# Kernel optimization log

Hardware: AMD Instinct MI355X
Metric: run time of the kernel (lower is better)

## Reference

```python
import jax, jax.numpy as jnp
from jax import lax
import numpy as np

N_PATTS, D_PATTS, L_PATTS = 64, 16, 64
L_OUT = L_PATTS  # module sets l_out = l_patts in both branches
RHO = 0.1
W = RHO ** (1.0 / L_PATTS)  # per-step decay weight
BIG = 1e30  # stands in for +inf at DP boundaries (avoids inf*0 nans)


def _dtw_matrix(x, patts, w):
    """Weighted-DTW DP matrix.
    x: (B, d, T), patts: (P, d, L) -> D: (B, P, L, T)
    D[i,j] = dist[i,j] + w * min(D[i-1,j], D[i,j-1], D[i-1,j-1]),
    with out-of-range predecessors = +inf and D[0,0] = dist[0,0].
    dist is the euclidean distance between x[:, :, j] and patts[:, :, i].
    """
    B, d, T = x.shape
    P, _, L = patts.shape
    x2 = jnp.sum(x * x, axis=1)              # (B, T)
    p2 = jnp.sum(patts * patts, axis=1)      # (P, L)
    xp = jnp.einsum('bdt,pdl->btpl', x, patts)  # (B, T, P, L)
    sq = x2[:, :, None, None] + p2[None, None, :, :] - 2.0 * xp
    dist = jnp.sqrt(jnp.maximum(sq, 1e-12))  # (B, T, P, L)
    dist_t = jnp.transpose(dist, (1, 0, 2, 3))  # (T, B, P, L) scan over time

    def col_step(prev_col, d_col):
        # prev_col = D[:, j-1] of shape (B, P, L); d_col = dist column (B, P, L)
        shifted = jnp.concatenate(
            [jnp.full_like(prev_col[..., :1], BIG), prev_col[..., :-1]], axis=-1)
        c = jnp.minimum(prev_col, shifted)  # min(D[i,j-1], D[i-1,j-1]) per i

        def cell(d_prev, inp):
            dist_i, c_i = inp              # each (B, P)
            m = jnp.minimum(d_prev, c_i)   # min over the 3 predecessors
            val = dist_i + jnp.where(m >= BIG * 0.5, 0.0, w * m)
            return val, val

        init = jnp.full(prev_col.shape[:2], BIG, prev_col.dtype)  # D[-1, j]
        _, col = lax.scan(
            cell, init,
            (jnp.moveaxis(d_col, -1, 0), jnp.moveaxis(c, -1, 0)))  # over i
        col = jnp.moveaxis(col, 0, -1)  # (B, P, L)
        return col, col

    init_col = jnp.full((B, P, L), BIG, dist.dtype)  # D[:, -1] = inf
    _, cols = lax.scan(col_step, init_col, dist_t)   # (T, B, P, L)
    return jnp.transpose(cols, (1, 2, 3, 0))         # (B, P, L, T)


def setup_inputs() -> dict:
    key = jax.random.key(0)
    kx, kp = jax.random.split(key)
    x = jax.random.normal(kx, (16, D_PATTS, 1024), dtype=jnp.float32)
    patts = jax.random.normal(kp, (N_PATTS, D_PATTS, L_PATTS), dtype=jnp.float32)
    return {"x": x, "patts": patts}


def reference(x, patts):
    D = _dtw_matrix(x, patts, W)          # (B, P, L, T)
    return D[:, :, :, -L_OUT:]            # last l_out time steps
```

## Files before the change

### kernel.cpp

```cpp
#include <hip/hip_runtime.h>
#include <math.h>

typedef _Float16 half8 __attribute__((ext_vector_type(8)));
typedef _Float16 h2 __attribute__((ext_vector_type(2)));
typedef float    f32x4 __attribute__((ext_vector_type(4)));
typedef unsigned int u32;
typedef unsigned long long u64;
typedef unsigned short u16;

#define BIGV 1e30f
#define RSTR 37

__device__ __forceinline__ u32 dpp_shr1(u32 oldv, u32 src) {
  return (u32)__builtin_amdgcn_update_dpp((int)oldv, (int)src, 0x138, 0xF, 0xF, false);
}
__device__ __forceinline__ float cvtlo(u32 v) {
  union { u16 u; _Float16 h; } c; c.u = (u16)v; return (float)c.h;
}
__device__ __forceinline__ u16 f2h(float f) {
  union { _Float16 h; u16 u; } c; c.h = (_Float16)f; return c.u;
}
__device__ __forceinline__ u32 pkrtz(float a, float b) {
  auto v = __builtin_amdgcn_cvt_pkrtz(a, b);
  union { decltype(v) h; u32 u; } c; c.h = v; return c.u;
}
__device__ __forceinline__ u32 funnel16(u32 hi, u32 lo, u32 sh) {
  return (u32)(((((u64)hi) << 32) | (u64)lo) >> sh);
}
__device__ __forceinline__ h2 as_h2(u32 u) { union { u32 u; h2 h; } x; x.u = u; return x.h; }

__global__ __launch_bounds__(512) void dtw_pc2(
    const float* __restrict__ x,
    const float* __restrict__ patts,
    float* __restrict__ out,
    float w) {
  __shared__ uint4 xsq[2050];
  __shared__ uint2 ring2[4 * 64 * RSTR];
  __shared__ float obuf[4 * 1024];
  __shared__ u16   x2h16[1024];

  const int tid = threadIdx.x, lane = tid & 63, wv = tid >> 6;
  const int b = blockIdx.x >> 4, pg = blockIdx.x & 15;
  const int role = wv >> 2, pr = wv & 3;
  const int p = pg * 4 + pr;
  const int le = lane & 15, kq = lane >> 4;

  {
    const float* xb = x + b * (16 * 1024);
    u16* xh = (u16*)xsq;
    for (int idx = tid; idx < 16384; idx += 512) {
      int d = idx >> 10, t = idx & 1023;
      xh[t * 16 + d] = f2h(xb[idx]);
    }
    if (tid == 0) { xsq[2048] = make_uint4(0,0,0,0); xsq[2049] = make_uint4(0,0,0,0); }
    __syncthreads();
    for (int t = tid; t < 1024; t += 512) {
      uint4 a0 = xsq[2 * t], a1 = xsq[2 * t + 1];
      float s2 = __builtin_amdgcn_fdot2(as_h2(a0.x), as_h2(a0.x), 0.f, false);
      s2 = __builtin_amdgcn_fdot2(as_h2(a0.y), as_h2(a0.y), s2, false);
      s2 = __builtin_amdgcn_fdot2(as_h2(a0.z), as_h2(a0.z), s2, false);
      s2 = __builtin_amdgcn_fdot2(as_h2(a0.w), as_h2(a0.w), s2, false);
      s2 = __builtin_amdgcn_fdot2(as_h2(a1.x), as_h2(a1.x), s2, false);
      s2 = __builtin_amdgcn_fdot2(as_h2(a1.y), as_h2(a1.y), s2, false);
      s2 = __builtin_amdgcn_fdot2(as_h2(a1.z), as_h2(a1.z), s2, false);
      s2 = __builtin_amdgcn_fdot2(as_h2(a1.w), as_h2(a1.w), s2, false);
      x2h16[t] = f2h(s2);
    }
  }
  __syncthreads();

  if (role == 0) {
    half8 bf[4];
    {
      const float* pp = patts + p * (16 * 64);
#pragma unroll
      for (int nb = 0; nb < 4; ++nb) {
        float pv[8]; float part = 0.f;
#pragma unroll
        for (int j = 0; j < 8; ++j) {
          float f = (kq < 2) ? pp[(8 * kq + j) * 64 + nb * 16 + le] : 0.f;
          pv[j] = f; part = fmaf(f, f, part);
        }
        part += __shfl_xor(part, 16, 64);
        part += __shfl_xor(part, 32, 64);
        u32 wd0 = pkrtz(-2.f * pv[0], -2.f * pv[1]);
        u32 wd1 = pkrtz(-2.f * pv[2], -2.f * pv[3]);
        u32 wd2 = pkrtz(-2.f * pv[4], -2.f * pv[5]);
        u32 wd3 = pkrtz(-2.f * pv[6], -2.f * pv[7]);
        if (kq == 2) { wd0 = 0x3C00u | ((u32)f2h(part) << 16); wd1 = 0; wd2 = 0; wd3 = 0; }
        union { uint4 q; half8 h; } bu; bu.q = make_uint4(wd0, wd1, wd2, wd3);
        bf[nb] = bu.h;
      }
    }
    int colp = 8 * kq;
    const int wpbase = pr * (64 * RSTR) + RSTR * le;

#define PRODUCE(T0) { \
    int aidx_ = (kq < 2) ? (2 * ((T0) + le) + kq) : 2048; \
    uint4 aq_ = xsq[aidx_]; \
    u32 x2b_ = (u32)x2h16[(T0) + le]; \
    aq_.x = (kq == 2) ? (x2b_ | 0x3C000000u) : aq_.x; \
    union { uint4 q; half8 h; } au_; au_.q = aq_; \
    int wb_ = wpbase + (colp >> 3); \
    bool mir_ = colp < 32; \
    _Pragma("unroll") \
    for (int nb_ = 0; nb_ < 4; ++nb_) { \
      f32x4 c_ = {0.f, 0.f, 0.f, 0.f}; \
      c_ = __builtin_amdgcn_mfma_f32_16x16x32_f16(au_.h, bf[nb_], c_, 0, 0, 0); \
      float d0_ = __builtin_amdgcn_sqrtf(fmaxf(c_[0], 1e-12f)); \
      float d1_ = __builtin_amdgcn_sqrtf(fmaxf(c_[1], 1e-12f)); \
      float d2_ = __builtin_amdgcn_sqrtf(fmaxf(c_[2], 1e-12f)); \
      float d3_ = __builtin_amdgcn_sqrtf(fmaxf(c_[3], 1e-12f)); \
      uint2 st_; st_.x = pkrtz(d0_, d1_); st_.y = pkrtz(d2_, d3_); \
      ring2[wb_ + (16 * RSTR) * nb_] = st_; \
      if (mir_) ring2[wb_ + (16 * RSTR) * nb_ + 32] = st_; \
    } \
    colp = (colp + 32) & 255; }

    PRODUCE(0); PRODUCE(16); PRODUCE(32); PRODUCE(48);
    __syncthreads();
#pragma unroll 1
    for (int k = 0; k < 30; ++k) {
      PRODUCE(32 * k + 64);
      PRODUCE(32 * k + 80);
      __syncthreads();
    }
    __syncthreads(); __syncthreads(); __syncthreads(); __syncthreads();

  } else {
    const int rcbase = pr * (64 * RSTR) + RSTR * lane;
    int colc = (((0 - lane) >> 2) << 3) & 255;
    const int ph = (0 - lane) & 3;
    const u32 shv = (u32)((ph & 1) * 16);
    const bool sel2 = (ph & 2) != 0;
    float prev = BIGV, shA = BIGV, shB = BIGV;
    const int bigbits = __float_as_int(BIGV);
    float* obf = obuf + pr * 1024;
    float* obw = obf + lane * 16;
    float* oprow = out + ((b * 64 + p) * 64 + lane) * 64;
    int nextq = 240;

#define LOADQ(Q0,Q1,Q2,Q3,Q4) { int ci_ = rcbase + (colc >> 3); \
    Q0 = ring2[ci_];     Q1 = ring2[ci_ + 1]; Q2 = ring2[ci_ + 2]; \
    Q3 = ring2[ci_ + 3]; Q4 = ring2[ci_ + 4]; \
    colc = (colc + 32) & 255; }

#define SHIFT(curv) { shB = shA; \
    shA = __int_as_float((int)dpp_shr1((u32)bigbits, (u32)__float_as_int(curv))); \
    prev = (curv); }

#define STEP_PRO(S, D) { float dist_ = (D); \
    float m_ = fminf(fminf(prev, shA), shB); \
    float ms_ = (m_ >= 0.5e30f) ? 0.f : m_; \
    float val_ = fmaf(w, ms_, dist_); \
    int t_ = (S) - lane; float cur_ = (t_ >= 0) ? val_ : BIGV; \
    SHIFT(cur_); }

#define STEP_MAIN(S, D) { float dist_ = (D); \
    float m_ = fminf(fminf(prev, shA), shB); \
    float cur_ = fmaf(w, m_, dist_); \
    SHIFT(cur_); }

#define STEP_EPI(S, D) { float dist_ = (D); \
    float m_ = fminf(fminf(prev, shA), shB); \
    float val_ = fmaf(w, m_, dist_); \
    int t_ = (S) - lane; float cur_ = (t_ <= 1023) ? val_ : BIGV; \
    if ((u32)(t_ - 960) < 64u) obw[t_ & 15] = val_; \
    SHIFT(cur_); }

#define FLUSHQ(SQ) { \
    if (nextq < 256 && 4 * nextq + 3 <= (SQ) - 1 - lane - 4) { \
      float4 v_ = *(const float4*)&obf[lane * 16 + ((nextq & 3) << 2)]; \
      *(float4*)(oprow + (nextq << 2) - 960) = v_; ++nextq; \
    } }

#define EXTRACT8(Q0, Q1, Q2, Q3, Q4) \
    u32 W0_ = sel2 ? Q0.y : Q0.x, W1_ = sel2 ? Q1.x : Q0.y, \
        W2_ = sel2 ? Q1.y : Q1.x, W3_ = sel2 ? Q2.x : Q1.y, \
        W4_ = sel2 ? Q2.y : Q2.x, W5_ = sel2 ? Q3.x : Q2.y, \
        W6_ = sel2 ? Q3.y : Q3.x, W7_ = sel2 ? Q4.x : Q3.y, \
        W8_ = sel2 ? Q4.y : Q4.x; \
    u32 A0 = funnel16(W1_, W0_, shv), A1 = funnel16(W2_, W1_, shv), \
        A2 = funnel16(W3_, W2_, shv), A3 = funnel16(W4_, W3_, shv), \
        A4 = funnel16(W5_, W4_, shv), A5 = funnel16(W6_, W5_, shv), \
        A6 = funnel16(W7_, W6_, shv), A7 = funnel16(W8_, W7_, shv);

#define S16(S0, STP) \
    STP((S0)+0,  cvtlo(A0)); STP((S0)+1,  cvtlo(A0 >> 16)); \
    STP((S0)+2,  cvtlo(A1)); STP((S0)+3,  cvtlo(A1 >> 16)); \
    STP((S0)+4,  cvtlo(A2)); STP((S0)+5,  cvtlo(A2 >> 16)); \
    STP((S0)+6,  cvtlo(A3)); STP((S0)+7,  cvtlo(A3 >> 16)); \
    STP((S0)+8,  cvtlo(A4)); STP((S0)+9,  cvtlo(A4 >> 16)); \
    STP((S0)+10, cvtlo(A5)); STP((S0)+11, cvtlo(A5 >> 16)); \
    STP((S0)+12, cvtlo(A6)); STP((S0)+13, cvtlo(A6 >> 16)); \
    STP((S0)+14, cvtlo(A7)); STP((S0)+15, cvtlo(A7 >> 16));

#define SET_PRO(S0)  S16(S0, STEP_PRO)
#define SET_MAIN(S0) S16(S0, STEP_MAIN)
#define SET_EPI(S0) \
    FLUSHQ((S0)+0);  STEP_EPI((S0)+0,  cvtlo(A0)); STEP_EPI((S0)+1,  cvtlo(A0 >> 16)); \
                     STEP_EPI((S0)+2,  cvtlo(A1)); STEP_EPI((S0)+3,  cvtlo(A1 >> 16)); \
    FLUSHQ((S0)+4);  STEP_EPI((S0)+4,  cvtlo(A2)); STEP_EPI((S0)+5,  cvtlo(A2 >> 16)); \
                     STEP_EPI((S0)+6,  cvtlo(A3)); STEP_EPI((S0)+7,  cvtlo(A3 >> 16)); \
    FLUSHQ((S0)+8);  STEP_EPI((S0)+8,  cvtlo(A4)); STEP_EPI((S0)+9,  cvtlo(A4 >> 16)); \
                     STEP_EPI((S0)+10, cvtlo(A5)); STEP_EPI((S0)+11, cvtlo(A5 >> 16)); \
    FLUSHQ((S0)+12); STEP_EPI((S0)+12, cvtlo(A6)); STEP_EPI((S0)+13, cvtlo(A6 >> 16)); \
                     STEP_EPI((S0)+14, cvtlo(A7)); STEP_EPI((S0)+15, cvtlo(A7 >> 16));

#define PHASE(C0,C1,C2,C3,C4,C5,C6,C7,C8,C9, L0,L1,L2,L3,L4,L5,L6,L7,L8,L9, S0, SETM) { \
    LOADQ(L0,L1,L2,L3,L4); LOADQ(L5,L6,L7,L8,L9); \
    { EXTRACT8(C0,C1,C2,C3,C4); SETM(S0); } \
    { EXTRACT8(C5,C6,C7,C8,C9); SETM((S0)+16); } \
    __syncthreads(); }

    __syncthreads();
    uint2 a0,a1,a2,a3,a4,a5,a6,a7,a8,a9;
    uint2 b0,b1,b2,b3,b4,b5,b6,b7,b8,b9;
    LOADQ(a0,a1,a2,a3,a4); LOADQ(a5,a6,a7,a8,a9);

    PHASE(a0,a1,a2,a3,a4,a5,a6,a7,a8,a9, b0,b1,b2,b3,b4,b5,b6,b7,b8,b9, 0,  SET_PRO);
    PHASE(b0,b1,b2,b3,b4,b5,b6,b7,b8,b9, a0,a1,a2,a3,a4,a5,a6,a7,a8,a9, 32, SET_PRO);
#pragma unroll 1
    for (int j = 1; j < 15; ++j) {
      PHASE(a0,a1,a2,a3,a4,a5,a6,a7,a8,a9, b0,b1,b2,b3,b4,b5,b6,b7,b8,b9, 64*j,      SET_MAIN);
      PHASE(b0,b1,b2,b3,b4,b5,b6,b7,b8,b9, a0,a1,a2,a3,a4,a5,a6,a7,a8,a9, 64*j + 32, SET_MAIN);
    }
    PHASE(a0,a1,a2,a3,a4,a5,a6,a7,a8,a9, b0,b1,b2,b3,b4,b5,b6,b7,b8,b9, 960,  SET_EPI);
    PHASE(b0,b1,b2,b3,b4,b5,b6,b7,b8,b9, a0,a1,a2,a3,a4,a5,a6,a7,a8,a9, 992,  SET_EPI);
    PHASE(a0,a1,a2,a3,a4,a5,a6,a7,a8,a9, b0,b1,b2,b3,b4,b5,b6,b7,b8,b9, 1024, SET_EPI);
    PHASE(b0,b1,b2,b3,b4,b5,b6,b7,b8,b9, a0,a1,a2,a3,a4,a5,a6,a7,a8,a9, 1056, SET_EPI);

#pragma unroll
    for (int rr = 0; rr < 4; ++rr) {
      if (nextq < 256) {
        float4 v_ = *(const float4*)&obf[lane * 16 + ((nextq & 3) << 2)];
        *(float4*)(oprow + (nextq << 2) - 960) = v_; ++nextq;
      }
    }
  }
}

extern "C" void kernel_launch(void* const* d_in, const int* in_sizes, int n_in,
                              void* d_out, int out_size, void* d_ws, size_t ws_size,
                              hipStream_t stream) {
  const float* x     = (const float*)d_in[0];
  const float* patts = (const float*)d_in[1];
  float* out         = (float*)d_out;
  const float w = (float)exp(log(0.1) / 64.0);
  dim3 grid(256), block(512);
  hipLaunchKernelGGL(dtw_pc2, grid, block, 0, stream, x, patts, out, w);
}
```

Baseline: 44.77 us.

## Process two DTW rows per lane with pair-packed ring layout

Restructures the consumer wavefront so each lane advances two time steps per DP step on an anti-diagonal. The ring buffer is re-laid-out as a byte-addressed row-pair ring with wraparound pointers, which removes the funnel-shift and select extraction. Output is now written directly to global memory instead of being staged through an LDS obuf, and plain barriers replace syncthreads. This is meant to cut ALU and LDS overhead per cell and halve the number of phases. The cost is a longer dependent chain per step and a larger ring footprint in LDS.

```diff
diff --git a/kernel.cpp b/kernel.cpp
--- a/kernel.cpp
+++ b/kernel.cpp
@@ -5,11 +5,9 @@
 typedef _Float16 h2 __attribute__((ext_vector_type(2)));
 typedef float    f32x4 __attribute__((ext_vector_type(4)));
 typedef unsigned int u32;
-typedef unsigned long long u64;
 typedef unsigned short u16;
 
 #define BIGV 1e30f
-#define RSTR 37
 
 __device__ __forceinline__ u32 dpp_shr1(u32 oldv, u32 src) {
   return (u32)__builtin_amdgcn_update_dpp((int)oldv, (int)src, 0x138, 0xF, 0xF, false);
@@ -24,20 +22,16 @@
   auto v = __builtin_amdgcn_cvt_pkrtz(a, b);
   union { decltype(v) h; u32 u; } c; c.h = v; return c.u;
 }
-__device__ __forceinline__ u32 funnel16(u32 hi, u32 lo, u32 sh) {
-  return (u32)(((((u64)hi) << 32) | (u64)lo) >> sh);
-}
 __device__ __forceinline__ h2 as_h2(u32 u) { union { u32 u; h2 h; } x; x.u = u; return x.h; }
 
-__global__ __launch_bounds__(512) void dtw_pc2(
+__global__ __launch_bounds__(512) void dtw_pc3(
     const float* __restrict__ x,
     const float* __restrict__ patts,
     float* __restrict__ out,
-    float w) {
+    float wd) {
   __shared__ uint4 xsq[2050];
-  __shared__ uint2 ring2[4 * 64 * RSTR];
-  __shared__ float obuf[4 * 1024];
   __shared__ u16   x2h16[1024];
+  __shared__ uint2 ring2[4 * 64 * 57];
 
   const int tid = threadIdx.x, lane = tid & 63, wv = tid >> 6;
   const int b = blockIdx.x >> 4, pg = blockIdx.x & 15;
@@ -92,8 +86,15 @@
         bf[nb] = bu.h;
       }
     }
-    int colp = 8 * kq;
-    const int wpbase = pr * (64 * RSTR) + RSTR * le;
+    u32 Aa[4], Ee[4];
+    const u32 pairbase = (u32)(pr * 29184);
+#pragma unroll
+    for (int nb = 0; nb < 4; ++nb) {
+      int row = nb * 16 + le;
+      u32 rb = pairbase + (u32)(row * 456);
+      Aa[nb] = rb + (u32)(4 * (2 * kq + (row & ~1)));
+      Ee[nb] = rb + 448u;
+    }
 
 #define PRODUCE(T0) { \
     int aidx_ = (kq < 2) ? (2 * ((T0) + le) + kq) : 2048; \
@@ -101,8 +102,6 @@
     u32 x2b_ = (u32)x2h16[(T0) + le]; \
     aq_.x = (kq == 2) ? (x2b_ | 0x3C000000u) : aq_.x; \
     union { uint4 q; half8 h; } au_; au_.q = aq_; \
-    int wb_ = wpbase + (colp >> 3); \
-    bool mir_ = colp < 32; \
     _Pragma("unroll") \
     for (int nb_ = 0; nb_ < 4; ++nb_) { \
       f32x4 c_ = {0.f, 0.f, 0.f, 0.f}; \
@@ -112,10 +111,9 @@
       float d2_ = __builtin_amdgcn_sqrtf(fmaxf(c_[2], 1e-12f)); \
       float d3_ = __builtin_amdgcn_sqrtf(fmaxf(c_[3], 1e-12f)); \
       uint2 st_; st_.x = pkrtz(d0_, d1_); st_.y = pkrtz(d2_, d3_); \
-      ring2[wb_ + (16 * RSTR) * nb_] = st_; \
-      if (mir_) ring2[wb_ + (16 * RSTR) * nb_ + 32] = st_; \
-    } \
-    colp = (colp + 32) & 255; }
+      *(uint2*)((char*)ring2 + Aa[nb_]) = st_; \
+      Aa[nb_] += 32u; if (Aa[nb_] >= Ee[nb_]) Aa[nb_] -= 448u; \
+    } }
 
     PRODUCE(0); PRODUCE(16); PRODUCE(32); PRODUCE(48);
     __syncthreads();
@@ -125,118 +123,81 @@
       PRODUCE(32 * k + 80);
       __syncthreads();
     }
-    __syncthreads(); __syncthreads(); __syncthreads(); __syncthreads();
+    for (int k = 0; k < 6; ++k) __syncthreads();
 
   } else {
-    const int rcbase = pr * (64 * RSTR) + RSTR * lane;
-    int colc = (((0 - lane) >> 2) << 3) & 255;
-    const int ph = (0 - lane) & 3;
-    const u32 shv = (u32)((ph & 1) * 16);
-    const bool sel2 = (ph & 2) != 0;
-    float prev = BIGV, shA = BIGV, shB = BIGV;
+    char* crow = (char*)ring2 + pr * 29184 + lane * 456;
+    u32 cb = 0;
+    const bool oddl = (lane & 1) != 0;
+    float prevB = BIGV, sA = BIGV, sB = BIGV, sBo = BIGV;
     const int bigbits = __float_as_int(BIGV);
-    float* obf = obuf + pr * 1024;
-    float* obw = obf + lane * 16;
     float* oprow = out + ((b * 64 + p) * 64 + lane) * 64;
-    int nextq = 240;
-
-#define LOADQ(Q0,Q1,Q2,Q3,Q4) { int ci_ = rcbase + (colc >> 3); \
-    Q0 = ring2[ci_];     Q1 = ring2[ci_ + 1]; Q2 = ring2[ci_ + 2]; \
-    Q3 = ring2[ci_ + 3]; Q4 = ring2[ci_ + 4]; \
-    colc = (colc + 32) & 255; }
-
-#define SHIFT(curv) { shB = shA; \
-    shA = __int_as_float((int)dpp_shr1((u32)bigbits, (u32)__float_as_int(curv))); \
-    prev = (curv); }
-
-#define STEP_PRO(S, D) { float dist_ = (D); \
-    float m_ = fminf(fminf(prev, shA), shB); \
-    float ms_ = (m_ >= 0.5e30f) ? 0.f : m_; \
-    float val_ = fmaf(w, ms_, dist_); \
-    int t_ = (S) - lane; float cur_ = (t_ >= 0) ? val_ : BIGV; \
-    SHIFT(cur_); }
-
-#define STEP_MAIN(S, D) { float dist_ = (D); \
-    float m_ = fminf(fminf(prev, shA), shB); \
-    float cur_ = fmaf(w, m_, dist_); \
-    SHIFT(cur_); }
-
-#define STEP_EPI(S, D) { float dist_ = (D); \
-    float m_ = fminf(fminf(prev, shA), shB); \
-    float val_ = fmaf(w, m_, dist_); \
-    int t_ = (S) - lane; float cur_ = (t_ <= 1023) ? val_ : BIGV; \
-    if ((u32)(t_ - 960) < 64u) obw[t_ & 15] = val_; \
-    SHIFT(cur_); }
-
-#define FLUSHQ(SQ) { \
-    if (nextq < 256 && 4 * nextq + 3 <= (SQ) - 1 - lane - 4) { \
-      float4 v_ = *(const float4*)&obf[lane * 16 + ((nextq & 3) << 2)]; \
-      *(float4*)(oprow + (nextq << 2) - 960) = v_; ++nextq; \
-    } }
-
-#define EXTRACT8(Q0, Q1, Q2, Q3, Q4) \
-    u32 W0_ = sel2 ? Q0.y : Q0.x, W1_ = sel2 ? Q1.x : Q0.y, \
-        W2_ = sel2 ? Q1.y : Q1.x, W3_ = sel2 ? Q2.x : Q1.y, \
-        W4_ = sel2 ? Q2.y : Q2.x, W5_ = sel2 ? Q3.x : Q2.y, \
-        W6_ = sel2 ? Q3.y : Q3.x, W7_ = sel2 ? Q4.x : Q3.y, \
-        W8_ = sel2 ? Q4.y : Q4.x; \
-    u32 A0 = funnel16(W1_, W0_, shv), A1 = funnel16(W2_, W1_, shv), \
-        A2 = funnel16(W3_, W2_, shv), A3 = funnel16(W4_, W3_, shv), \
-        A4 = funnel16(W5_, W4_, shv), A5 = funnel16(W6_, W5_, shv), \
-        A6 = funnel16(W7_, W6_, shv), A7 = funnel16(W8_, W7_, shv);
-
-#define S16(S0, STP) \
-    STP((S0)+0,  cvtlo(A0)); STP((S0)+1,  cvtlo(A0 >> 16)); \
-    STP((S0)+2,  cvtlo(A1)); STP((S0)+3,  cvtlo(A1 >> 16)); \
-    STP((S0)+4,  cvtlo(A2)); STP((S0)+5,  cvtlo(A2 >> 16)); \
-    STP((S0)+6,  cvtlo(A3)); STP((S0)+7,  cvtlo(A3 >> 16)); \
-    STP((S0)+8,  cvtlo(A4)); STP((S0)+9,  cvtlo(A4 >> 16)); \
-    STP((S0)+10, cvtlo(A5)); STP((S0)+11, cvtlo(A5 >> 16)); \
-    STP((S0)+12, cvtlo(A6)); STP((S0)+13, cvtlo(A6 >> 16)); \
-    STP((S0)+14, cvtlo(A7)); STP((S0)+15, cvtlo(A7 >> 16));
-
-#define SET_PRO(S0)  S16(S0, STEP_PRO)
-#define SET_MAIN(S0) S16(S0, STEP_MAIN)
-#define SET_EPI(S0) \
-    FLUSHQ((S0)+0);  STEP_EPI((S0)+0,  cvtlo(A0)); STEP_EPI((S0)+1,  cvtlo(A0 >> 16)); \
-                     STEP_EPI((S0)+2,  cvtlo(A1)); STEP_EPI((S0)+3,  cvtlo(A1 >> 16)); \
-    FLUSHQ((S0)+4);  STEP_EPI((S0)+4,  cvtlo(A2)); STEP_EPI((S0)+5,  cvtlo(A2 >> 16)); \
-                     STEP_EPI((S0)+6,  cvtlo(A3)); STEP_EPI((S0)+7,  cvtlo(A3 >> 16)); \
-    FLUSHQ((S0)+8);  STEP_EPI((S0)+8,  cvtlo(A4)); STEP_EPI((S0)+9,  cvtlo(A4 >> 16)); \
-                     STEP_EPI((S0)+10, cvtlo(A5)); STEP_EPI((S0)+11, cvtlo(A5 >> 16)); \
-    FLUSHQ((S0)+12); STEP_EPI((S0)+12, cvtlo(A6)); STEP_EPI((S0)+13, cvtlo(A6 >> 16)); \
-                     STEP_EPI((S0)+14, cvtlo(A7)); STEP_EPI((S0)+15, cvtlo(A7 >> 16));
-
-#define PHASE(C0,C1,C2,C3,C4,C5,C6,C7,C8,C9, L0,L1,L2,L3,L4,L5,L6,L7,L8,L9, S0, SETM) { \
-    LOADQ(L0,L1,L2,L3,L4); LOADQ(L5,L6,L7,L8,L9); \
-    { EXTRACT8(C0,C1,C2,C3,C4); SETM(S0); } \
-    { EXTRACT8(C5,C6,C7,C8,C9); SETM((S0)+16); } \
-    __syncthreads(); }
-
-    __syncthreads();
-    uint2 a0,a1,a2,a3,a4,a5,a6,a7,a8,a9;
-    uint2 b0,b1,b2,b3,b4,b5,b6,b7,b8,b9;
-    LOADQ(a0,a1,a2,a3,a4); LOADQ(a5,a6,a7,a8,a9);
-
-    PHASE(a0,a1,a2,a3,a4,a5,a6,a7,a8,a9, b0,b1,b2,b3,b4,b5,b6,b7,b8,b9, 0,  SET_PRO);
-    PHASE(b0,b1,b2,b3,b4,b5,b6,b7,b8,b9, a0,a1,a2,a3,a4,a5,a6,a7,a8,a9, 32, SET_PRO);
+    float* ps = oprow;
+    uint2 C0,C1,C2,C3,C4,C5,C6,C7, N0,N1,N2,N3,N4,N5,N6,N7;
+    uint2 carry; carry.x = 0; carry.y = 0;
+
+#define DPSTEP(K, WRD, PM, EP) { \
+    u32 wrd_ = (WRD); \
+    float d0_ = cvtlo(wrd_); float d1_ = cvtlo(wrd_ >> 16); \
+    float mA_ = fminf(fminf(prevB, sA), sBo); \
+    if (PM) mA_ = (mA_ >= 0.5e30f) ? 0.f : mA_; \
+    float vA_ = fmaf(wd, mA_, d0_); \
+    float mB_ = fminf(fminf(vA_, sB), sA); \
+    float vB_ = fmaf(wd, mB_, d1_); \
+    if (PM) { bool act_ = ((K) >= lane); vA_ = act_ ? vA_ : BIGV; vB_ = act_ ? vB_ : BIGV; } \
+    if (EP) { if ((u32)((K) - lane - 480) < 32u) \
+        *(float2*)(ps + 2 * ((K) & 15)) = make_float2(vA_, vB_); } \
+    sBo = sB; \
+    sA = __int_as_float((int)dpp_shr1((u32)bigbits, (u32)__float_as_int(vA_))); \
+    sB = __int_as_float((int)dpp_shr1((u32)bigbits, (u32)__float_as_int(vB_))); \
+    prevB = vB_; }
+
+#define PAIR2(K2, CJ, CJM1, PM, EP) { \
+    u32 w0_ = oddl ? (CJM1).y : (CJ).x; \
+    u32 w1_ = oddl ? (CJ).x   : (CJ).y; \
+    DPSTEP((K2),     w0_, PM, EP); \
+    DPSTEP((K2) + 1, w1_, PM, EP); }
+
+#define CLOAD(Q0,Q1,Q2,Q3,Q4,Q5,Q6,Q7) { \
+    char* na_ = crow + cb; \
+    Q0 = *(uint2*)(na_);      Q1 = *(uint2*)(na_ + 8); \
+    Q2 = *(uint2*)(na_ + 16); Q3 = *(uint2*)(na_ + 24); \
+    Q4 = *(uint2*)(na_ + 32); Q5 = *(uint2*)(na_ + 40); \
+    Q6 = *(uint2*)(na_ + 48); Q7 = *(uint2*)(na_ + 56); \
+    cb += 64; if (cb == 448) cb = 0; }
+
+#define PHASE(A0_,A1_,A2_,A3_,A4_,A5_,A6_,A7_, B0_,B1_,B2_,B3_,B4_,B5_,B6_,B7_, K0, PM, EP) { \
+    if (EP) ps = oprow + (2 * (K0) - 960) - 2 * lane; \
+    CLOAD(B0_,B1_,B2_,B3_,B4_,B5_,B6_,B7_); \
+    PAIR2((K0) + 0,  A0_, carry, PM, EP); \
+    PAIR2((K0) + 2,  A1_, A0_,   PM, EP); \
+    PAIR2((K0) + 4,  A2_, A1_,   PM, EP); \
+    PAIR2((K0) + 6,  A3_, A2_,   PM, EP); \
+    PAIR2((K0) + 8,  A4_, A3_,   PM, EP); \
+    PAIR2((K0) + 10, A5_, A4_,   PM, EP); \
+    PAIR2((K0) + 12, A6_, A5_,   PM, EP); \
+    PAIR2((K0) + 14, A7_, A6_,   PM, EP); \
+    carry = A7_; \
+    __builtin_amdgcn_s_barrier(); }
+
+    __builtin_amdgcn_s_barrier();
+    CLOAD(C0,C1,C2,C3,C4,C5,C6,C7);
+
+    PHASE(C0,C1,C2,C3,C4,C5,C6,C7, N0,N1,N2,N3,N4,N5,N6,N7, 0,  1, 0);
+    PHASE(N0,N1,N2,N3,N4,N5,N6,N7, C0,C1,C2,C3,C4,C5,C6,C7, 16, 1, 0);
+    PHASE(C0,C1,C2,C3,C4,C5,C6,C7, N0,N1,N2,N3,N4,N5,N6,N7, 32, 1, 0);
+    PHASE(N0,N1,N2,N3,N4,N5,N6,N7, C0,C1,C2,C3,C4,C5,C6,C7, 48, 1, 0);
 #pragma unroll 1
-    for (int j = 1; j < 15; ++j) {
-      PHASE(a0,a1,a2,a3,a4,a5,a6,a7,a8,a9, b0,b1,b2,b3,b4,b5,b6,b7,b8,b9, 64*j,      SET_MAIN);
-      PHASE(b0,b1,b2,b3,b4,b5,b6,b7,b8,b9, a0,a1,a2,a3,a4,a5,a6,a7,a8,a9, 64*j + 32, SET_MAIN);
-    }
-    PHASE(a0,a1,a2,a3,a4,a5,a6,a7,a8,a9, b0,b1,b2,b3,b4,b5,b6,b7,b8,b9, 960,  SET_EPI);
-    PHASE(b0,b1,b2,b3,b4,b5,b6,b7,b8,b9, a0,a1,a2,a3,a4,a5,a6,a7,a8,a9, 992,  SET_EPI);
-    PHASE(a0,a1,a2,a3,a4,a5,a6,a7,a8,a9, b0,b1,b2,b3,b4,b5,b6,b7,b8,b9, 1024, SET_EPI);
-    PHASE(b0,b1,b2,b3,b4,b5,b6,b7,b8,b9, a0,a1,a2,a3,a4,a5,a6,a7,a8,a9, 1056, SET_EPI);
-
-#pragma unroll
-    for (int rr = 0; rr < 4; ++rr) {
-      if (nextq < 256) {
-        float4 v_ = *(const float4*)&obf[lane * 16 + ((nextq & 3) << 2)];
-        *(float4*)(oprow + (nextq << 2) - 960) = v_; ++nextq;
-      }
-    }
+    for (int j = 2; j < 15; ++j) {
+      PHASE(C0,C1,C2,C3,C4,C5,C6,C7, N0,N1,N2,N3,N4,N5,N6,N7, 32 * j,      0, 0);
+      PHASE(N0,N1,N2,N3,N4,N5,N6,N7, C0,C1,C2,C3,C4,C5,C6,C7, 32 * j + 16, 0, 0);
+    }
+    PHASE(C0,C1,C2,C3,C4,C5,C6,C7, N0,N1,N2,N3,N4,N5,N6,N7, 480, 0, 1);
+    PHASE(N0,N1,N2,N3,N4,N5,N6,N7, C0,C1,C2,C3,C4,C5,C6,C7, 496, 0, 1);
+    PHASE(C0,C1,C2,C3,C4,C5,C6,C7, N0,N1,N2,N3,N4,N5,N6,N7, 512, 0, 1);
+    PHASE(N0,N1,N2,N3,N4,N5,N6,N7, C0,C1,C2,C3,C4,C5,C6,C7, 528, 0, 1);
+    PHASE(C0,C1,C2,C3,C4,C5,C6,C7, N0,N1,N2,N3,N4,N5,N6,N7, 544, 0, 1);
+    PHASE(N0,N1,N2,N3,N4,N5,N6,N7, C0,C1,C2,C3,C4,C5,C6,C7, 560, 0, 1);
   }
 }
 
@@ -248,5 +209,5 @@
   float* out         = (float*)d_out;
   const float w = (float)exp(log(0.1) / 64.0);
   dim3 grid(256), block(512);
-  hipLaunchKernelGGL(dtw_pc2, grid, block, 0, stream, x, patts, out, w);
-}
+  hipLaunchKernelGGL(dtw_pc3, grid, block, 0, stream, x, patts, out, w);
+}
```

New measurement: 44.26 us. About the same (-1.1%).

## Halve patterns per block, double grid, and store epilogue outputs directly

Applied to the files above, without the earlier changes.

Each block now handles 2 patterns instead of 4 (256 threads, 512 blocks), giving more blocks across the CUs and a smaller shared-memory footprint per block. The epilogue drops the LDS output staging buffer and its queued float4 flush, and instead writes pairs of results straight to global memory as float2 stores. The ring stride changes from 37 to 36, which may affect LDS bank conflicts. The trade-off is that each block repeats the x load and fp16 conversion for fewer patterns, and the direct global stores are narrower and issued from inside the dependent DP chain.

```diff
diff --git a/kernel.cpp b/kernel.cpp
--- a/kernel.cpp
+++ b/kernel.cpp
@@ -9,7 +9,7 @@
 typedef unsigned short u16;
 
 #define BIGV 1e30f
-#define RSTR 37
+#define RSTR 36
 
 __device__ __forceinline__ u32 dpp_shr1(u32 oldv, u32 src) {
   return (u32)__builtin_amdgcn_update_dpp((int)oldv, (int)src, 0x138, 0xF, 0xF, false);
@@ -29,32 +29,31 @@
 }
 __device__ __forceinline__ h2 as_h2(u32 u) { union { u32 u; h2 h; } x; x.u = u; return x.h; }
 
-__global__ __launch_bounds__(512) void dtw_pc2(
+__global__ __launch_bounds__(256) void dtw_pc4(
     const float* __restrict__ x,
     const float* __restrict__ patts,
     float* __restrict__ out,
     float w) {
   __shared__ uint4 xsq[2050];
-  __shared__ uint2 ring2[4 * 64 * RSTR];
-  __shared__ float obuf[4 * 1024];
+  __shared__ uint2 ring2[2 * 64 * RSTR];
   __shared__ u16   x2h16[1024];
 
   const int tid = threadIdx.x, lane = tid & 63, wv = tid >> 6;
-  const int b = blockIdx.x >> 4, pg = blockIdx.x & 15;
-  const int role = wv >> 2, pr = wv & 3;
-  const int p = pg * 4 + pr;
+  const int b = blockIdx.x >> 5, pg = blockIdx.x & 31;
+  const int role = wv >> 1, pr = wv & 1;
+  const int p = pg * 2 + pr;
   const int le = lane & 15, kq = lane >> 4;
 
   {
     const float* xb = x + b * (16 * 1024);
     u16* xh = (u16*)xsq;
-    for (int idx = tid; idx < 16384; idx += 512) {
+    for (int idx = tid; idx < 16384; idx += 256) {
       int d = idx >> 10, t = idx & 1023;
       xh[t * 16 + d] = f2h(xb[idx]);
     }
     if (tid == 0) { xsq[2048] = make_uint4(0,0,0,0); xsq[2049] = make_uint4(0,0,0,0); }
     __syncthreads();
-    for (int t = tid; t < 1024; t += 512) {
+    for (int t = tid; t < 1024; t += 256) {
       uint4 a0 = xsq[2 * t], a1 = xsq[2 * t + 1];
       float s2 = __builtin_amdgcn_fdot2(as_h2(a0.x), as_h2(a0.x), 0.f, false);
       s2 = __builtin_amdgcn_fdot2(as_h2(a0.y), as_h2(a0.y), s2, false);
@@ -133,12 +132,9 @@
     const int ph = (0 - lane) & 3;
     const u32 shv = (u32)((ph & 1) * 16);
     const bool sel2 = (ph & 2) != 0;
-    float prev = BIGV, shA = BIGV, shB = BIGV;
+    float prev = BIGV, shA = BIGV, shB = BIGV, pend = 0.f;
     const int bigbits = __float_as_int(BIGV);
-    float* obf = obuf + pr * 1024;
-    float* obw = obf + lane * 16;
     float* oprow = out + ((b * 64 + p) * 64 + lane) * 64;
-    int nextq = 240;
 
 #define LOADQ(Q0,Q1,Q2,Q3,Q4) { int ci_ = rcbase + (colc >> 3); \
     Q0 = ring2[ci_];     Q1 = ring2[ci_ + 1]; Q2 = ring2[ci_ + 2]; \
@@ -165,14 +161,10 @@
     float m_ = fminf(fminf(prev, shA), shB); \
     float val_ = fmaf(w, m_, dist_); \
     int t_ = (S) - lane; float cur_ = (t_ <= 1023) ? val_ : BIGV; \
-    if ((u32)(t_ - 960) < 64u) obw[t_ & 15] = val_; \
+    if ((t_ & 1) == 0) { pend = val_; } \
+    else if ((u32)(t_ - 961) < 63u) { \
+      *(float2*)(oprow + (t_ - 961)) = make_float2(pend, val_); } \
     SHIFT(cur_); }
-
-#define FLUSHQ(SQ) { \
-    if (nextq < 256 && 4 * nextq + 3 <= (SQ) - 1 - lane - 4) { \
-      float4 v_ = *(const float4*)&obf[lane * 16 + ((nextq & 3) << 2)]; \
-      *(float4*)(oprow + (nextq << 2) - 960) = v_; ++nextq; \
-    } }
 
 #define EXTRACT8(Q0, Q1, Q2, Q3, Q4) \
     u32 W0_ = sel2 ? Q0.y : Q0.x, W1_ = sel2 ? Q1.x : Q0.y, \
@@ -197,15 +189,7 @@
 
 #define SET_PRO(S0)  S16(S0, STEP_PRO)
 #define SET_MAIN(S0) S16(S0, STEP_MAIN)
-#define SET_EPI(S0) \
-    FLUSHQ((S0)+0);  STEP_EPI((S0)+0,  cvtlo(A0)); STEP_EPI((S0)+1,  cvtlo(A0 >> 16)); \
-                     STEP_EPI((S0)+2,  cvtlo(A1)); STEP_EPI((S0)+3,  cvtlo(A1 >> 16)); \
-    FLUSHQ((S0)+4);  STEP_EPI((S0)+4,  cvtlo(A2)); STEP_EPI((S0)+5,  cvtlo(A2 >> 16)); \
-                     STEP_EPI((S0)+6,  cvtlo(A3)); STEP_EPI((S0)+7,  cvtlo(A3 >> 16)); \
-    FLUSHQ((S0)+8);  STEP_EPI((S0)+8,  cvtlo(A4)); STEP_EPI((S0)+9,  cvtlo(A4 >> 16)); \
-                     STEP_EPI((S0)+10, cvtlo(A5)); STEP_EPI((S0)+11, cvtlo(A5 >> 16)); \
-    FLUSHQ((S0)+12); STEP_EPI((S0)+12, cvtlo(A6)); STEP_EPI((S0)+13, cvtlo(A6 >> 16)); \
-                     STEP_EPI((S0)+14, cvtlo(A7)); STEP_EPI((S0)+15, cvtlo(A7 >> 16));
+#define SET_EPI(S0)  S16(S0, STEP_EPI)
 
 #define PHASE(C0,C1,C2,C3,C4,C5,C6,C7,C8,C9, L0,L1,L2,L3,L4,L5,L6,L7,L8,L9, S0, SETM) { \
     LOADQ(L0,L1,L2,L3,L4); LOADQ(L5,L6,L7,L8,L9); \
@@ -229,14 +213,6 @@
     PHASE(b0,b1,b2,b3,b4,b5,b6,b7,b8,b9, a0,a1,a2,a3,a4,a5,a6,a7,a8,a9, 992,  SET_EPI);
     PHASE(a0,a1,a2,a3,a4,a5,a6,a7,a8,a9, b0,b1,b2,b3,b4,b5,b6,b7,b8,b9, 1024, SET_EPI);
     PHASE(b0,b1,b2,b3,b4,b5,b6,b7,b8,b9, a0,a1,a2,a3,a4,a5,a6,a7,a8,a9, 1056, SET_EPI);
-
-#pragma unroll
-    for (int rr = 0; rr < 4; ++rr) {
-      if (nextq < 256) {
-        float4 v_ = *(const float4*)&obf[lane * 16 + ((nextq & 3) << 2)];
-        *(float4*)(oprow + (nextq << 2) - 960) = v_; ++nextq;
-      }
-    }
   }
 }
 
@@ -247,6 +223,6 @@
   const float* patts = (const float*)d_in[1];
   float* out         = (float*)d_out;
   const float w = (float)exp(log(0.1) / 64.0);
-  dim3 grid(256), block(512);
-  hipLaunchKernelGGL(dtw_pc2, grid, block, 0, stream, x, patts, out, w);
-}
+  dim3 grid(512), block(256);
+  hipLaunchKernelGGL(dtw_pc4, grid, block, 0, stream, x, patts, out, w);
+}
```

Result: slower. 51.57 us (+15.2%).
